# Kernel tuning notes

Measured on AMD Instinct MI355X. Metric: run time of the kernel, lower is better.

The kernel has to match this reference:

```python
import jax, jax.numpy as jnp
import numpy as np

_ALPHA_REF = 0.95
_L_REF = 96.0
GATE_THRESH = 0.7
EPS = 1e-12


def setup_inputs() -> dict:
    key = jax.random.key(0)
    ks = jax.random.split(key, 6)
    B, L, d_model = 16, 2048, 1024
    d_half = d_model // 2
    s = 1.0 / np.sqrt(d_model)
    return {
        "x": jax.random.normal(ks[0], (B, L, d_model), dtype=jnp.float32),
        "W_sem": jax.random.normal(ks[1], (d_half, d_model), dtype=jnp.float32) * s,
        "W_epi": jax.random.normal(ks[2], (d_half, d_model), dtype=jnp.float32) * s,
        "null_w": jax.random.normal(ks[3], (1, d_model), dtype=jnp.float32) * s,
        "null_b": jnp.zeros((1,), dtype=jnp.float32),
        "out_w": jax.random.normal(ks[4], (d_model, d_model), dtype=jnp.float32) * s,
        "out_b": jnp.zeros((d_model,), dtype=jnp.float32),
    }


def _normalize(v):
    # torch F.normalize: v / max(||v||, eps)
    n = jnp.linalg.norm(v, axis=-1, keepdims=True)
    return v / jnp.maximum(n, EPS)


def reference(x, W_sem, W_epi, null_w, null_b, out_w, out_b):
    B, L, d_model = x.shape
    d_half = d_model // 2
    a = _ALPHA_REF ** (_L_REF / L)  # length-adaptive EMA coefficient

    # Precompute key projections for the write steps 0..L-2: (L-1, B, d_half)
    ks_all = jnp.einsum("bld,hd->lbh", x[:, :-1, :], W_sem)
    ke_all = jnp.einsum("bld,hd->lbh", x[:, :-1, :], W_epi)
    w_all = (jnp.arange(1, L, dtype=x.dtype)) / L  # recency weights (t+1)/L

    def step(carry, inp):
        M_sem, M_epi = carry  # each (B, d_half, d_half)
        ks_t, ke_t, w_t = inp
        kns = _normalize(ks_t)
        kne = _normalize(ke_t)
        vps = jnp.einsum("bij,bj->bi", M_sem, kns)
        vpe = jnp.einsum("bij,bj->bi", M_epi, kne)
        err_s = jnp.linalg.norm(ks_t - vps, axis=-1)
        err_e = jnp.linalg.norm(ke_t - vpe, axis=-1)
        ref_s = GATE_THRESH * jnp.linalg.norm(ks_t, axis=-1)
        ref_e = GATE_THRESH * jnp.linalg.norm(ke_t, axis=-1)
        fire = ((err_s >= ref_s) | (err_e >= ref_e)).astype(x.dtype)  # (B,)
        g3 = fire[:, None, None]
        Delta_s = (ks_t - vps)[:, :, None] * kns[:, None, :]  # rank-1 outer product
        Delta_e = (ke_t - vpe)[:, :, None] * kne[:, None, :]
        M_sem = M_sem + (1.0 - a) * g3 * Delta_s
        M_epi = M_epi + (1.0 - a) * w_t * g3 * Delta_e
        return (M_sem, M_epi), None

    M0 = jnp.zeros((B, d_half, d_half), dtype=x.dtype)
    (M_sem, M_epi), _ = jax.lax.scan(step, (M0, M0), (ks_all, ke_all, w_all))

    # Query retrieval at position L-1
    q = x[:, -1, :]
    qns = _normalize(q @ W_sem.T)
    qne = _normalize(q @ W_epi.T)
    r_sem = jnp.einsum("bij,bj->bi", M_sem, qns)
    r_epi = jnp.einsum("bij,bj->bi", M_epi, qne)
    r = jnp.concatenate([r_sem, r_epi], axis=-1)  # (B, d_model)
    g_null = jax.nn.sigmoid(q @ null_w.T + null_b)  # (B, 1)
    r = g_null * r
    return r @ out_w.T + out_b
```

## Files before the change

### kernel.cpp

```cpp
#include <hip/hip_runtime.h>
#include <math.h>

#define B_    16
#define L_    2048
#define LM1   2047
#define D_    1024
#define H_    512
#define TBLK  64
#define NBLK  32

__global__ void k_proj(const float* __restrict__ x, const float* __restrict__ Wsem,
                       const float* __restrict__ Wepi, float* __restrict__ K)
{
    __shared__ float As[16][68];
    __shared__ float Bs[16][68];
    const int tid = threadIdx.x;
    const int tx = tid & 15, ty = tid >> 4;
    const int r0 = blockIdx.x * 64;
    const int n0 = blockIdx.y * 64;
    const int lr  = tid >> 2;
    const int lk4 = (tid & 3) << 2;
    const int rowg = r0 + lr;
    const bool rok = rowg < B_ * LM1;
    const int rowc = rok ? rowg : 0;
    const int bb = rowc / LM1;
    const int tt = rowc - bb * LM1;
    const float* xrow = x + ((size_t)bb * L_ + tt) * D_;
    const int nW = n0 + lr;
    const float* wrow = (nW < H_) ? (Wsem + (size_t)nW * D_)
                                  : (Wepi + (size_t)(nW - H_) * D_);
    float acc[4][4];
#pragma unroll
    for (int i = 0; i < 4; ++i)
#pragma unroll
        for (int j = 0; j < 4; ++j) acc[i][j] = 0.f;

    for (int kk = 0; kk < D_; kk += 16) {
        const float4 av = rok ? *(const float4*)(xrow + kk + lk4) : make_float4(0.f,0.f,0.f,0.f);
        const float4 bv = *(const float4*)(wrow + kk + lk4);
        As[lk4+0][lr] = av.x; As[lk4+1][lr] = av.y; As[lk4+2][lr] = av.z; As[lk4+3][lr] = av.w;
        Bs[lk4+0][lr] = bv.x; Bs[lk4+1][lr] = bv.y; Bs[lk4+2][lr] = bv.z; Bs[lk4+3][lr] = bv.w;
        __syncthreads();
#pragma unroll
        for (int k = 0; k < 16; ++k) {
            const float4 a4 = *(const float4*)&As[k][ty << 2];
            const float4 b4 = *(const float4*)&Bs[k][tx << 2];
            const float aa[4] = {a4.x, a4.y, a4.z, a4.w};
            const float bbv[4] = {b4.x, b4.y, b4.z, b4.w};
#pragma unroll
            for (int i = 0; i < 4; ++i)
#pragma unroll
                for (int j = 0; j < 4; ++j)
                    acc[i][j] = fmaf(aa[i], bbv[j], acc[i][j]);
        }
        __syncthreads();
    }
#pragma unroll
    for (int i = 0; i < 4; ++i) {
        const int r = r0 + (ty << 2) + i;
        if (r < B_ * LM1)
            *(float4*)(K + (size_t)r * D_ + n0 + (tx << 2)) =
                make_float4(acc[i][0], acc[i][1], acc[i][2], acc[i][3]);
    }
}

__global__ void k_norms(const float* __restrict__ K, float* __restrict__ nk2,
                        float* __restrict__ rn)
{
    const int r = blockIdx.x;
    const int tid = threadIdx.x;
    const float4 v = *(const float4*)(K + (size_t)r * D_ + (tid << 2));
    float s = v.x*v.x + v.y*v.y + v.z*v.z + v.w*v.w;
#pragma unroll
    for (int o = 32; o; o >>= 1) s += __shfl_xor(s, o);
    __shared__ float part[4];
    const int wid = tid >> 6, lane = tid & 63;
    if (lane == 0) part[wid] = s;
    __syncthreads();
    if (tid == 0) {
        const int b = r / LM1, t = r - b * LM1;
        const float s0 = part[0] + part[1];
        const float s1 = part[2] + part[3];
        nk2[(size_t)(b*2+0)*LM1 + t] = s0;
        nk2[(size_t)(b*2+1)*LM1 + t] = s1;
        rn [(size_t)(b*2+0)*LM1 + t] = 1.f / fmaxf(sqrtf(s0), 1e-12f);
        rn [(size_t)(b*2+1)*LM1 + t] = 1.f / fmaxf(sqrtf(s1), 1e-12f);
    }
}

__global__ void k_gram(const float* __restrict__ K, const float* __restrict__ rn,
                       float* __restrict__ G)
{
    const int blk = blockIdx.x;
    const int bm  = blockIdx.y;
    const int b = bm >> 1, m = bm & 1;
    const int t0 = blk * TBLK;
    const int Tb = (LM1 - t0 < TBLK) ? (LM1 - t0) : TBLK;
    __shared__ float As[16][68];
    const int tid = threadIdx.x;
    const int tx = tid & 15, ty = tid >> 4;
    const int lr = tid >> 2, lk4 = (tid & 3) << 2;
    const float* Abase = K + ((size_t)(b * LM1 + t0)) * D_ + m * H_;
    float acc[4][4];
#pragma unroll
    for (int i = 0; i < 4; ++i)
#pragma unroll
        for (int j = 0; j < 4; ++j) acc[i][j] = 0.f;

    for (int kk = 0; kk < H_; kk += 16) {
        const float4 av = (lr < Tb) ? *(const float4*)(Abase + (size_t)lr * D_ + kk + lk4)
                                    : make_float4(0.f,0.f,0.f,0.f);
        As[lk4+0][lr] = av.x; As[lk4+1][lr] = av.y; As[lk4+2][lr] = av.z; As[lk4+3][lr] = av.w;
        __syncthreads();
#pragma unroll
        for (int k = 0; k < 16; ++k) {
            const float4 a4 = *(const float4*)&As[k][ty << 2];
            const float4 b4 = *(const float4*)&As[k][tx << 2];
            const float aa[4] = {a4.x, a4.y, a4.z, a4.w};
            const float bbv[4] = {b4.x, b4.y, b4.z, b4.w};
#pragma unroll
            for (int i = 0; i < 4; ++i)
#pragma unroll
                for (int j = 0; j < 4; ++j)
                    acc[i][j] = fmaf(aa[i], bbv[j], acc[i][j]);
        }
        __syncthreads();
    }
    const float* rnb = rn + (size_t)bm * LM1 + t0;
    float* Gout = G + ((size_t)bm * NBLK + blk) * (TBLK * TBLK);
#pragma unroll
    for (int i = 0; i < 4; ++i) {
        const int t = (ty << 2) + i;
        const float rt = (t < Tb) ? rnb[t] : 0.f;
#pragma unroll
        for (int j = 0; j < 4; ++j) {
            const int s = (tx << 2) + j;
            const int d = s - t;
            if (d >= 0) {
                const float val = (t < Tb && s < Tb) ? rt * rnb[s] * acc[i][j] : 0.f;
                Gout[(size_t)t * TBLK + d] = val;
            }
        }
    }
}

__global__ void k_vext(const float* __restrict__ K, const float* __restrict__ M,
                       const float* __restrict__ rn, float* __restrict__ Vext,
                       int t0, int Tb)
{
    const int bm = blockIdx.y;
    const int b = bm >> 1, m = bm & 1;
    const int n0 = blockIdx.x * 64;
    __shared__ float As[16][68];
    __shared__ float Bs[16][68];
    const int tid = threadIdx.x;
    const int tx = tid & 15, ty = tid >> 4;
    const int lr = tid >> 2, lk4 = (tid & 3) << 2;
    const float* Abase = K + ((size_t)(b * LM1 + t0)) * D_ + m * H_;
    const float* Bbase = M + (size_t)bm * H_ * H_;
    float acc[4][4];
#pragma unroll
    for (int i = 0; i < 4; ++i)
#pragma unroll
        for (int j = 0; j < 4; ++j) acc[i][j] = 0.f;

    for (int kk = 0; kk < H_; kk += 16) {
        const float4 av = (lr < Tb) ? *(const float4*)(Abase + (size_t)lr * D_ + kk + lk4)
                                    : make_float4(0.f,0.f,0.f,0.f);
        const float4 bv = *(const float4*)(Bbase + (size_t)(n0 + lr) * H_ + kk + lk4);
        As[lk4+0][lr] = av.x; As[lk4+1][lr] = av.y; As[lk4+2][lr] = av.z; As[lk4+3][lr] = av.w;
        Bs[lk4+0][lr] = bv.x; Bs[lk4+1][lr] = bv.y; Bs[lk4+2][lr] = bv.z; Bs[lk4+3][lr] = bv.w;
        __syncthreads();
#pragma unroll
        for (int k = 0; k < 16; ++k) {
            const float4 a4 = *(const float4*)&As[k][ty << 2];
            const float4 b4 = *(const float4*)&Bs[k][tx << 2];
            const float aa[4] = {a4.x, a4.y, a4.z, a4.w};
            const float bbv[4] = {b4.x, b4.y, b4.z, b4.w};
#pragma unroll
            for (int i = 0; i < 4; ++i)
#pragma unroll
                for (int j = 0; j < 4; ++j)
                    acc[i][j] = fmaf(aa[i], bbv[j], acc[i][j]);
        }
        __syncthreads();
    }
    const float* rnb = rn + (size_t)bm * LM1 + t0;
#pragma unroll
    for (int i = 0; i < 4; ++i) {
        const int t = (ty << 2) + i;
        if (t < Tb) {
            const float rv = rnb[t];
            *(float4*)(Vext + ((size_t)bm * TBLK + t) * H_ + n0 + (tx << 2)) =
                make_float4(rv*acc[i][0], rv*acc[i][1], rv*acc[i][2], rv*acc[i][3]);
        }
    }
}

__global__ void __launch_bounds__(512) k_seq(
    const float* __restrict__ K, const float* __restrict__ Vext,
    const float* __restrict__ G, const float* __restrict__ nk2,
    float* __restrict__ AU, int t0, int Tb, int blk, float omA)
{
    const int b = blockIdx.x;
    const int tid = threadIdx.x;
    const int wid = tid >> 6, lane = tid & 63;
    __shared__ float Gsh[2 * TBLK * TBLK];
    __shared__ float part[32];
    {
        const float4* s0 = (const float4*)(G + ((size_t)(b*2+0) * NBLK + blk) * (TBLK*TBLK));
        const float4* s1 = (const float4*)(G + ((size_t)(b*2+1) * NBLK + blk) * (TBLK*TBLK));
        float4* dst = (float4*)Gsh;
        dst[tid]        = s0[tid];
        dst[tid + 512]  = s0[tid + 512];
        dst[tid + 1024] = s1[tid];
        dst[tid + 1536] = s1[tid + 512];
    }
    float p0[TBLK], p1[TBLK];
#pragma unroll
    for (int i = 0; i < TBLK; ++i) { p0[i] = 0.f; p1[i] = 0.f; }
    __syncthreads();

    const float* Kb0 = K + ((size_t)(b * LM1 + t0)) * D_ + tid;
    const float* Kb1 = Kb0 + H_;
    const float* Vb0 = Vext + ((size_t)(b*2+0) * TBLK) * H_ + tid;
    const float* Vb1 = Vext + ((size_t)(b*2+1) * TBLK) * H_ + tid;
    float* AU0 = AU + ((size_t)(b*2+0) * TBLK) * H_ + tid;
    float* AU1 = AU + ((size_t)(b*2+1) * TBLK) * H_ + tid;
    const float* q0 = nk2 + (size_t)(b*2+0) * LM1 + t0;
    const float* q1 = nk2 + (size_t)(b*2+1) * LM1 + t0;

    float kc0 = Kb0[0], kc1 = Kb1[0], vc0 = Vb0[0], vc1 = Vb1[0];
    float n0c = q0[0],  n1c = q1[0];

    for (int t = 0; t < Tb; ++t) {
        const float u0 = kc0 - vc0 - p0[0];
        const float u1 = kc1 - vc1 - p1[0];
        float kn0 = 0.f, kn1 = 0.f, vn0 = 0.f, vn1 = 0.f, nn0 = 0.f, nn1 = 0.f;
        if (t + 1 < Tb) {
            kn0 = Kb0[(size_t)(t+1) * D_]; kn1 = Kb1[(size_t)(t+1) * D_];
            vn0 = Vb0[(t+1) * H_];         vn1 = Vb1[(t+1) * H_];
            nn0 = q0[t+1];                 nn1 = q1[t+1];
        }
        float s0 = u0 * u0, s1 = u1 * u1;
#pragma unroll
        for (int o = 32; o; o >>= 1) { s0 += __shfl_xor(s0, o); s1 += __shfl_xor(s1, o); }
        float* pp = &part[(t & 1) << 4];
        if (lane == 0) { pp[wid] = s0; pp[wid + 8] = s1; }
        __syncthreads();
        float Ns = 0.f, Ne = 0.f;
#pragma unroll
        for (int i = 0; i < 8; ++i) { Ns += pp[i]; Ne += pp[i + 8]; }
        const bool fire = (Ns >= 0.49f * n0c) || (Ne >= 0.49f * n1c);
        const float w = (float)(t0 + t + 1) * (1.0f / (float)L_);
        const float vv0 = fire ? omA * u0 : 0.f;
        const float vv1 = fire ? omA * w * u1 : 0.f;
        AU0[(size_t)t * H_] = vv0;
        AU1[(size_t)t * H_] = vv1;
        const float* g0 = Gsh + t * TBLK;
        const float* g1 = Gsh + (TBLK + t) * TBLK;
        if (fire) {
#pragma unroll
            for (int q = 0; q < 16; ++q) {
                const float4 a = ((const float4*)g0)[q];
                const float4 c = ((const float4*)g1)[q];
                const int d0 = q << 2;
                if (q > 0) { p0[d0-1] = fmaf(a.x, vv0, p0[d0]); p1[d0-1] = fmaf(c.x, vv1, p1[d0]); }
                p0[d0+0] = fmaf(a.y, vv0, p0[d0+1]);  p1[d0+0] = fmaf(c.y, vv1, p1[d0+1]);
                p0[d0+1] = fmaf(a.z, vv0, p0[d0+2]);  p1[d0+1] = fmaf(c.z, vv1, p1[d0+2]);
                p0[d0+2] = fmaf(a.w, vv0, p0[d0+3]);  p1[d0+2] = fmaf(c.w, vv1, p1[d0+3]);
            }
        } else {
#pragma unroll
            for (int d = 1; d < TBLK; ++d) { p0[d-1] = p0[d]; p1[d-1] = p1[d]; }
        }
        p0[TBLK-1] = 0.f; p1[TBLK-1] = 0.f;
        kc0 = kn0; kc1 = kn1; vc0 = vn0; vc1 = vn1; n0c = nn0; n1c = nn1;
    }
}

__global__ void k_update(const float* __restrict__ AU, const float* __restrict__ K,
                         const float* __restrict__ rn, float* __restrict__ M,
                         int t0, int Tb)
{
    const int bm = blockIdx.y;
    const int b = bm >> 1, m = bm & 1;
    const int i0 = (blockIdx.x >> 3) * 64;
    const int j0 = (blockIdx.x & 7) * 64;
    __shared__ float As[16][68];
    __shared__ float Bs[16][68];
    const int tid = threadIdx.x;
    const int tx = tid & 15, ty = tid >> 4;
    const int lk = tid >> 4;
    const int lc4 = (tid & 15) << 2;
    float acc[4][4];
#pragma unroll
    for (int i = 0; i < 4; ++i)
#pragma unroll
        for (int j = 0; j < 4; ++j) acc[i][j] = 0.f;

    for (int kk = 0; kk < TBLK; kk += 16) {
        const int kt = kk + lk;
        const bool ok = kt < Tb;
        float4 av = ok ? *(const float4*)(AU + ((size_t)bm * TBLK + kt) * H_ + i0 + lc4)
                       : make_float4(0.f,0.f,0.f,0.f);
        const float rv = ok ? rn[(size_t)bm * LM1 + t0 + kt] : 0.f;
        float4 bv = ok ? *(const float4*)(K + ((size_t)(b * LM1 + t0 + kt)) * D_ + m * H_ + j0 + lc4)
                       : make_float4(0.f,0.f,0.f,0.f);
        bv.x *= rv; bv.y *= rv; bv.z *= rv; bv.w *= rv;
        *(float4*)&As[lk][lc4] = av;
        *(float4*)&Bs[lk][lc4] = bv;
        __syncthreads();
#pragma unroll
        for (int k = 0; k < 16; ++k) {
            const float4 a4 = *(const float4*)&As[k][ty << 2];
            const float4 b4 = *(const float4*)&Bs[k][tx << 2];
            const float aa[4] = {a4.x, a4.y, a4.z, a4.w};
            const float bbv[4] = {b4.x, b4.y, b4.z, b4.w};
#pragma unroll
            for (int i = 0; i < 4; ++i)
#pragma unroll
                for (int j = 0; j < 4; ++j)
                    acc[i][j] = fmaf(aa[i], bbv[j], acc[i][j]);
        }
        __syncthreads();
    }
#pragma unroll
    for (int i = 0; i < 4; ++i) {
        float4* p = (float4*)(M + ((size_t)bm * H_ + i0 + (ty << 2) + i) * H_ + j0 + (tx << 2));
        float4 old = *p;
        old.x += acc[i][0]; old.y += acc[i][1]; old.z += acc[i][2]; old.w += acc[i][3];
        *p = old;
    }
}

__global__ void __launch_bounds__(1024) k_q(
    const float* __restrict__ x, const float* __restrict__ Wsem,
    const float* __restrict__ Wepi, const float* __restrict__ nw,
    const float* __restrict__ nb, float* __restrict__ qn, float* __restrict__ gnull)
{
    const int b = blockIdx.x, tid = threadIdx.x;
    __shared__ float qsh[D_];
    __shared__ float red[16];
    qsh[tid] = x[((size_t)b * L_ + (L_ - 1)) * D_ + tid];
    __syncthreads();
    const float* wrow = (tid < H_) ? (Wsem + (size_t)tid * D_)
                                   : (Wepi + (size_t)(tid - H_) * D_);
    float s = 0.f;
    for (int d = 0; d < D_; d += 4) {
        const float4 w4 = *(const float4*)(wrow + d);
        s += qsh[d]*w4.x + qsh[d+1]*w4.y + qsh[d+2]*w4.z + qsh[d+3]*w4.w;
    }
    float sq = s * s;
#pragma unroll
    for (int o = 32; o; o >>= 1) sq += __shfl_xor(sq, o);
    const int wid = tid >> 6, lane = tid & 63;
    if (lane == 0) red[wid] = sq;
    __syncthreads();
    float n2s = 0.f, n2e = 0.f;
#pragma unroll
    for (int i = 0; i < 8; ++i) { n2s += red[i]; n2e += red[i + 8]; }
    const float rns = 1.f / fmaxf(sqrtf(n2s), 1e-12f);
    const float rne = 1.f / fmaxf(sqrtf(n2e), 1e-12f);
    qn[(size_t)b * D_ + tid] = s * ((tid < H_) ? rns : rne);
    if (wid == 0) {
        float g = 0.f;
        for (int d = lane * 4; d < D_; d += 256) {
            const float4 w4 = *(const float4*)(nw + d);
            g += qsh[d]*w4.x + qsh[d+1]*w4.y + qsh[d+2]*w4.z + qsh[d+3]*w4.w;
        }
#pragma unroll
        for (int o = 32; o; o >>= 1) g += __shfl_xor(g, o);
        if (lane == 0) gnull[b] = 1.f / (1.f + expf(-(g + nb[0])));
    }
}

__global__ void k_rmv(const float* __restrict__ M, const float* __restrict__ qn,
                      const float* __restrict__ gnull, float* __restrict__ rg)
{
    const int b = blockIdx.x;
    const int n = blockIdx.y * 4 + (threadIdx.x >> 6);
    const int lane = threadIdx.x & 63;
    const int m = n >> 9, i = n & 511;
    const float* Mr = M + ((size_t)(b*2+m) * H_ + i) * H_;
    const float* qv = qn + (size_t)b * D_ + m * H_;
    float s = 0.f;
#pragma unroll
    for (int it = 0; it < 2; ++it) {
        const int j = lane * 4 + it * 256;
        const float4 m4 = *(const float4*)(Mr + j);
        const float4 q4 = *(const float4*)(qv + j);
        s += m4.x*q4.x + m4.y*q4.y + m4.z*q4.z + m4.w*q4.w;
    }
#pragma unroll
    for (int o = 32; o; o >>= 1) s += __shfl_xor(s, o);
    if (lane == 0) rg[(size_t)b * D_ + n] = gnull[b] * s;
}

__global__ void k_out(const float* __restrict__ rg, const float* __restrict__ outw,
                      const float* __restrict__ outb, float* __restrict__ out)
{
    const int b = blockIdx.x;
    const int o = blockIdx.y * 4 + (threadIdx.x >> 6);
    const int lane = threadIdx.x & 63;
    const float* wr = outw + (size_t)o * D_;
    const float* rv = rg + (size_t)b * D_;
    float s = 0.f;
#pragma unroll
    for (int it = 0; it < 4; ++it) {
        const int j = lane * 4 + it * 256;
        const float4 w4 = *(const float4*)(wr + j);
        const float4 r4 = *(const float4*)(rv + j);
        s += w4.x*r4.x + w4.y*r4.y + w4.z*r4.z + w4.w*r4.w;
    }
#pragma unroll
    for (int o2 = 32; o2; o2 >>= 1) s += __shfl_xor(s, o2);
    if (lane == 0) out[(size_t)b * D_ + o] = s + outb[o];
}

extern "C" void kernel_launch(void* const* d_in, const int* in_sizes, int n_in,
                              void* d_out, int out_size, void* d_ws, size_t ws_size,
                              hipStream_t stream)
{
    (void)in_sizes; (void)n_in; (void)out_size;
    const float* x     = (const float*)d_in[0];
    const float* Wsem  = (const float*)d_in[1];
    const float* Wepi  = (const float*)d_in[2];
    const float* nullw = (const float*)d_in[3];
    const float* nullb = (const float*)d_in[4];
    const float* outw  = (const float*)d_in[5];
    const float* outb  = (const float*)d_in[6];
    float* out = (float*)d_out;

    float* ws = (float*)d_ws;
    size_t off = 0;
    float* K     = ws + off; off += (size_t)B_ * LM1 * D_;
    float* nk2   = ws + off; off += (size_t)B_ * 2 * LM1;
    float* rn    = ws + off; off += (size_t)B_ * 2 * LM1;
    float* Mm    = ws + off; off += (size_t)B_ * 2 * H_ * H_;
    float* Vext  = ws + off; off += (size_t)B_ * 2 * TBLK * H_;
    float* G     = ws + off; off += (size_t)B_ * 2 * NBLK * TBLK * TBLK;
    float* AU    = ws + off; off += (size_t)B_ * 2 * TBLK * H_;
    float* qn    = ws + off; off += (size_t)B_ * D_;
    float* gnull = ws + off; off += (size_t)B_;
    float* rg    = ws + off; off += (size_t)B_ * D_;
    if (ws_size < off * sizeof(float)) return;

    const float omA = (float)(1.0 - pow(0.95, 96.0 / 2048.0));

    hipMemsetAsync(Mm, 0, (size_t)B_ * 2 * H_ * H_ * sizeof(float), stream);

    k_proj <<<dim3(512, 16), 256, 0, stream>>>(x, Wsem, Wepi, K);
    k_norms<<<dim3(B_ * LM1), 256, 0, stream>>>(K, nk2, rn);
    k_gram <<<dim3(NBLK, B_ * 2), 256, 0, stream>>>(K, rn, G);

    for (int blk = 0; blk < NBLK; ++blk) {
        const int t0 = blk * TBLK;
        const int Tb = (LM1 - t0 < TBLK) ? (LM1 - t0) : TBLK;
        k_vext  <<<dim3(8, B_ * 2), 256, 0, stream>>>(K, Mm, rn, Vext, t0, Tb);
        k_seq   <<<dim3(B_), 512, 0, stream>>>(K, Vext, G, nk2, AU, t0, Tb, blk, omA);
        k_update<<<dim3(64, B_ * 2), 256, 0, stream>>>(AU, K, rn, Mm, t0, Tb);
    }

    k_q  <<<dim3(B_), 1024, 0, stream>>>(x, Wsem, Wepi, nullw, nullb, qn, gnull);
    k_rmv<<<dim3(16, 256), 256, 0, stream>>>(Mm, qn, gnull, rg);
    k_out<<<dim3(16, 256), 256, 0, stream>>>(rg, outw, outb, out);
}
```

Before: 7.000 ms.

## Fuse per-block vext/seq/update launches into one persistent cooperative kernel

Replaces the 96 per-chunk kernel launches (vext, seq, update across 32 chunks) and the memset with a single cooperative persistent kernel of 256 workgroups that uses grid.sync between phases. The vext GEMM is split-K across two 256-thread halves with a shared-memory reduction, and the update GEMM tiles are distributed across all workgroups. This removes launch overhead and inter-kernel gaps, at the cost of grid-wide barriers and only 16 workgroups being busy during the sequential phase.

```diff
diff --git a/kernel.cpp b/kernel.cpp
--- a/kernel.cpp
+++ b/kernel.cpp
@@ -1,5 +1,8 @@
 #include <hip/hip_runtime.h>
+#include <hip/hip_cooperative_groups.h>
 #include <math.h>
+
+namespace cg = cooperative_groups;
 
 #define B_    16
 #define L_    2048
@@ -8,6 +11,7 @@
 #define H_    512
 #define TBLK  64
 #define NBLK  32
+#define NWG   256
 
 __global__ void k_proj(const float* __restrict__ x, const float* __restrict__ Wsem,
                        const float* __restrict__ Wepi, float* __restrict__ K)
@@ -144,193 +148,224 @@
     }
 }
 
-__global__ void k_vext(const float* __restrict__ K, const float* __restrict__ M,
-                       const float* __restrict__ rn, float* __restrict__ Vext,
-                       int t0, int Tb)
-{
-    const int bm = blockIdx.y;
-    const int b = bm >> 1, m = bm & 1;
-    const int n0 = blockIdx.x * 64;
-    __shared__ float As[16][68];
-    __shared__ float Bs[16][68];
+__global__ void __launch_bounds__(512, 2) k_scan(
+    const float* __restrict__ K, const float* __restrict__ rn,
+    const float* __restrict__ nk2, const float* __restrict__ G,
+    float* __restrict__ Mm, float* __restrict__ Vext, float* __restrict__ AU,
+    float omA)
+{
+    cg::grid_group grid = cg::this_grid();
+    const int wg  = blockIdx.x;
     const int tid = threadIdx.x;
-    const int tx = tid & 15, ty = tid >> 4;
-    const int lr = tid >> 2, lk4 = (tid & 3) << 2;
-    const float* Abase = K + ((size_t)(b * LM1 + t0)) * D_ + m * H_;
-    const float* Bbase = M + (size_t)bm * H_ * H_;
-    float acc[4][4];
-#pragma unroll
-    for (int i = 0; i < 4; ++i)
-#pragma unroll
-        for (int j = 0; j < 4; ++j) acc[i][j] = 0.f;
-
-    for (int kk = 0; kk < H_; kk += 16) {
-        const float4 av = (lr < Tb) ? *(const float4*)(Abase + (size_t)lr * D_ + kk + lk4)
-                                    : make_float4(0.f,0.f,0.f,0.f);
-        const float4 bv = *(const float4*)(Bbase + (size_t)(n0 + lr) * H_ + kk + lk4);
-        As[lk4+0][lr] = av.x; As[lk4+1][lr] = av.y; As[lk4+2][lr] = av.z; As[lk4+3][lr] = av.w;
-        Bs[lk4+0][lr] = bv.x; Bs[lk4+1][lr] = bv.y; Bs[lk4+2][lr] = bv.z; Bs[lk4+3][lr] = bv.w;
-        __syncthreads();
-#pragma unroll
-        for (int k = 0; k < 16; ++k) {
-            const float4 a4 = *(const float4*)&As[k][ty << 2];
-            const float4 b4 = *(const float4*)&Bs[k][tx << 2];
-            const float aa[4] = {a4.x, a4.y, a4.z, a4.w};
-            const float bbv[4] = {b4.x, b4.y, b4.z, b4.w};
+    __shared__ float sh[8448];
+    __shared__ float part[32];
+
+    {
+        float4* M4 = (float4*)Mm;
+        for (int i = wg * 512 + tid; i < (B_*2*H_*H_) / 4; i += NWG * 512)
+            M4[i] = make_float4(0.f, 0.f, 0.f, 0.f);
+    }
+    grid.sync();
+
+    for (int blk = 0; blk < NBLK; ++blk) {
+        const int t0 = blk * TBLK;
+        const int Tb = (LM1 - t0 < TBLK) ? (LM1 - t0) : TBLK;
+
+        {
+            const int sub = tid >> 8, t256 = tid & 255;
+            float* As = sh + sub * 2176;
+            float* Bs = As + 1088;
+            float* Cred = sh + 4352;
+            const int bm = wg >> 3, n0 = (wg & 7) << 6;
+            const int b = bm >> 1, m = bm & 1;
+            const int tx = t256 & 15, ty = t256 >> 4;
+            const int lr = t256 >> 2, lk4 = (t256 & 3) << 2;
+            const float* Abase = K + ((size_t)(b * LM1 + t0)) * D_ + m * H_ + sub * 256;
+            const float* Bbase = Mm + (size_t)bm * H_ * H_ + sub * 256;
+            float acc[4][4];
 #pragma unroll
             for (int i = 0; i < 4; ++i)
 #pragma unroll
-                for (int j = 0; j < 4; ++j)
-                    acc[i][j] = fmaf(aa[i], bbv[j], acc[i][j]);
-        }
-        __syncthreads();
-    }
-    const float* rnb = rn + (size_t)bm * LM1 + t0;
-#pragma unroll
-    for (int i = 0; i < 4; ++i) {
-        const int t = (ty << 2) + i;
-        if (t < Tb) {
-            const float rv = rnb[t];
-            *(float4*)(Vext + ((size_t)bm * TBLK + t) * H_ + n0 + (tx << 2)) =
-                make_float4(rv*acc[i][0], rv*acc[i][1], rv*acc[i][2], rv*acc[i][3]);
-        }
-    }
-}
-
-__global__ void __launch_bounds__(512) k_seq(
-    const float* __restrict__ K, const float* __restrict__ Vext,
-    const float* __restrict__ G, const float* __restrict__ nk2,
-    float* __restrict__ AU, int t0, int Tb, int blk, float omA)
-{
-    const int b = blockIdx.x;
-    const int tid = threadIdx.x;
-    const int wid = tid >> 6, lane = tid & 63;
-    __shared__ float Gsh[2 * TBLK * TBLK];
-    __shared__ float part[32];
-    {
-        const float4* s0 = (const float4*)(G + ((size_t)(b*2+0) * NBLK + blk) * (TBLK*TBLK));
-        const float4* s1 = (const float4*)(G + ((size_t)(b*2+1) * NBLK + blk) * (TBLK*TBLK));
-        float4* dst = (float4*)Gsh;
-        dst[tid]        = s0[tid];
-        dst[tid + 512]  = s0[tid + 512];
-        dst[tid + 1024] = s1[tid];
-        dst[tid + 1536] = s1[tid + 512];
-    }
-    float p0[TBLK], p1[TBLK];
-#pragma unroll
-    for (int i = 0; i < TBLK; ++i) { p0[i] = 0.f; p1[i] = 0.f; }
-    __syncthreads();
-
-    const float* Kb0 = K + ((size_t)(b * LM1 + t0)) * D_ + tid;
-    const float* Kb1 = Kb0 + H_;
-    const float* Vb0 = Vext + ((size_t)(b*2+0) * TBLK) * H_ + tid;
-    const float* Vb1 = Vext + ((size_t)(b*2+1) * TBLK) * H_ + tid;
-    float* AU0 = AU + ((size_t)(b*2+0) * TBLK) * H_ + tid;
-    float* AU1 = AU + ((size_t)(b*2+1) * TBLK) * H_ + tid;
-    const float* q0 = nk2 + (size_t)(b*2+0) * LM1 + t0;
-    const float* q1 = nk2 + (size_t)(b*2+1) * LM1 + t0;
-
-    float kc0 = Kb0[0], kc1 = Kb1[0], vc0 = Vb0[0], vc1 = Vb1[0];
-    float n0c = q0[0],  n1c = q1[0];
-
-    for (int t = 0; t < Tb; ++t) {
-        const float u0 = kc0 - vc0 - p0[0];
-        const float u1 = kc1 - vc1 - p1[0];
-        float kn0 = 0.f, kn1 = 0.f, vn0 = 0.f, vn1 = 0.f, nn0 = 0.f, nn1 = 0.f;
-        if (t + 1 < Tb) {
-            kn0 = Kb0[(size_t)(t+1) * D_]; kn1 = Kb1[(size_t)(t+1) * D_];
-            vn0 = Vb0[(t+1) * H_];         vn1 = Vb1[(t+1) * H_];
-            nn0 = q0[t+1];                 nn1 = q1[t+1];
-        }
-        float s0 = u0 * u0, s1 = u1 * u1;
-#pragma unroll
-        for (int o = 32; o; o >>= 1) { s0 += __shfl_xor(s0, o); s1 += __shfl_xor(s1, o); }
-        float* pp = &part[(t & 1) << 4];
-        if (lane == 0) { pp[wid] = s0; pp[wid + 8] = s1; }
-        __syncthreads();
-        float Ns = 0.f, Ne = 0.f;
-#pragma unroll
-        for (int i = 0; i < 8; ++i) { Ns += pp[i]; Ne += pp[i + 8]; }
-        const bool fire = (Ns >= 0.49f * n0c) || (Ne >= 0.49f * n1c);
-        const float w = (float)(t0 + t + 1) * (1.0f / (float)L_);
-        const float vv0 = fire ? omA * u0 : 0.f;
-        const float vv1 = fire ? omA * w * u1 : 0.f;
-        AU0[(size_t)t * H_] = vv0;
-        AU1[(size_t)t * H_] = vv1;
-        const float* g0 = Gsh + t * TBLK;
-        const float* g1 = Gsh + (TBLK + t) * TBLK;
-        if (fire) {
-#pragma unroll
-            for (int q = 0; q < 16; ++q) {
-                const float4 a = ((const float4*)g0)[q];
-                const float4 c = ((const float4*)g1)[q];
-                const int d0 = q << 2;
-                if (q > 0) { p0[d0-1] = fmaf(a.x, vv0, p0[d0]); p1[d0-1] = fmaf(c.x, vv1, p1[d0]); }
-                p0[d0+0] = fmaf(a.y, vv0, p0[d0+1]);  p1[d0+0] = fmaf(c.y, vv1, p1[d0+1]);
-                p0[d0+1] = fmaf(a.z, vv0, p0[d0+2]);  p1[d0+1] = fmaf(c.z, vv1, p1[d0+2]);
-                p0[d0+2] = fmaf(a.w, vv0, p0[d0+3]);  p1[d0+2] = fmaf(c.w, vv1, p1[d0+3]);
-            }
-        } else {
-#pragma unroll
-            for (int d = 1; d < TBLK; ++d) { p0[d-1] = p0[d]; p1[d-1] = p1[d]; }
-        }
-        p0[TBLK-1] = 0.f; p1[TBLK-1] = 0.f;
-        kc0 = kn0; kc1 = kn1; vc0 = vn0; vc1 = vn1; n0c = nn0; n1c = nn1;
-    }
-}
-
-__global__ void k_update(const float* __restrict__ AU, const float* __restrict__ K,
-                         const float* __restrict__ rn, float* __restrict__ M,
-                         int t0, int Tb)
-{
-    const int bm = blockIdx.y;
-    const int b = bm >> 1, m = bm & 1;
-    const int i0 = (blockIdx.x >> 3) * 64;
-    const int j0 = (blockIdx.x & 7) * 64;
-    __shared__ float As[16][68];
-    __shared__ float Bs[16][68];
-    const int tid = threadIdx.x;
-    const int tx = tid & 15, ty = tid >> 4;
-    const int lk = tid >> 4;
-    const int lc4 = (tid & 15) << 2;
-    float acc[4][4];
-#pragma unroll
-    for (int i = 0; i < 4; ++i)
-#pragma unroll
-        for (int j = 0; j < 4; ++j) acc[i][j] = 0.f;
-
-    for (int kk = 0; kk < TBLK; kk += 16) {
-        const int kt = kk + lk;
-        const bool ok = kt < Tb;
-        float4 av = ok ? *(const float4*)(AU + ((size_t)bm * TBLK + kt) * H_ + i0 + lc4)
-                       : make_float4(0.f,0.f,0.f,0.f);
-        const float rv = ok ? rn[(size_t)bm * LM1 + t0 + kt] : 0.f;
-        float4 bv = ok ? *(const float4*)(K + ((size_t)(b * LM1 + t0 + kt)) * D_ + m * H_ + j0 + lc4)
-                       : make_float4(0.f,0.f,0.f,0.f);
-        bv.x *= rv; bv.y *= rv; bv.z *= rv; bv.w *= rv;
-        *(float4*)&As[lk][lc4] = av;
-        *(float4*)&Bs[lk][lc4] = bv;
-        __syncthreads();
-#pragma unroll
-        for (int k = 0; k < 16; ++k) {
-            const float4 a4 = *(const float4*)&As[k][ty << 2];
-            const float4 b4 = *(const float4*)&Bs[k][tx << 2];
-            const float aa[4] = {a4.x, a4.y, a4.z, a4.w};
-            const float bbv[4] = {b4.x, b4.y, b4.z, b4.w};
-#pragma unroll
-            for (int i = 0; i < 4; ++i)
-#pragma unroll
-                for (int j = 0; j < 4; ++j)
-                    acc[i][j] = fmaf(aa[i], bbv[j], acc[i][j]);
-        }
-        __syncthreads();
-    }
-#pragma unroll
-    for (int i = 0; i < 4; ++i) {
-        float4* p = (float4*)(M + ((size_t)bm * H_ + i0 + (ty << 2) + i) * H_ + j0 + (tx << 2));
-        float4 old = *p;
-        old.x += acc[i][0]; old.y += acc[i][1]; old.z += acc[i][2]; old.w += acc[i][3];
-        *p = old;
+                for (int j = 0; j < 4; ++j) acc[i][j] = 0.f;
+
+            for (int kk = 0; kk < 256; kk += 16) {
+                const float4 av = (lr < Tb) ? *(const float4*)(Abase + (size_t)lr * D_ + kk + lk4)
+                                            : make_float4(0.f,0.f,0.f,0.f);
+                const float4 bv = *(const float4*)(Bbase + (size_t)(n0 + lr) * H_ + kk + lk4);
+                As[(lk4+0)*68 + lr] = av.x; As[(lk4+1)*68 + lr] = av.y;
+                As[(lk4+2)*68 + lr] = av.z; As[(lk4+3)*68 + lr] = av.w;
+                Bs[(lk4+0)*68 + lr] = bv.x; Bs[(lk4+1)*68 + lr] = bv.y;
+                Bs[(lk4+2)*68 + lr] = bv.z; Bs[(lk4+3)*68 + lr] = bv.w;
+                __syncthreads();
+#pragma unroll
+                for (int k = 0; k < 16; ++k) {
+                    const float4 a4 = *(const float4*)&As[k*68 + (ty << 2)];
+                    const float4 b4 = *(const float4*)&Bs[k*68 + (tx << 2)];
+                    const float aa[4] = {a4.x, a4.y, a4.z, a4.w};
+                    const float bbv[4] = {b4.x, b4.y, b4.z, b4.w};
+#pragma unroll
+                    for (int i = 0; i < 4; ++i)
+#pragma unroll
+                        for (int j = 0; j < 4; ++j)
+                            acc[i][j] = fmaf(aa[i], bbv[j], acc[i][j]);
+                }
+                __syncthreads();
+            }
+            if (sub == 1) {
+#pragma unroll
+                for (int i = 0; i < 4; ++i)
+#pragma unroll
+                    for (int j = 0; j < 4; ++j)
+                        Cred[((size_t)((ty << 2) + i) << 6) + (tx << 2) + j] = acc[i][j];
+            }
+            __syncthreads();
+            if (sub == 0) {
+                const float* rnb = rn + (size_t)bm * LM1 + t0;
+#pragma unroll
+                for (int i = 0; i < 4; ++i) {
+                    const int t = (ty << 2) + i;
+                    if (t < Tb) {
+                        const float rv = rnb[t];
+                        const float* cr = &Cred[((size_t)t << 6) + (tx << 2)];
+                        *(float4*)(Vext + ((size_t)bm * TBLK + t) * H_ + n0 + (tx << 2)) =
+                            make_float4(rv*(acc[i][0]+cr[0]), rv*(acc[i][1]+cr[1]),
+                                        rv*(acc[i][2]+cr[2]), rv*(acc[i][3]+cr[3]));
+                    }
+                }
+            }
+        }
+        grid.sync();
+
+        if (wg < B_) {
+            const int b = wg;
+            const int wid = tid >> 6, lane = tid & 63;
+            {
+                const float4* s0 = (const float4*)(G + ((size_t)(b*2+0) * NBLK + blk) * (TBLK*TBLK));
+                const float4* s1 = (const float4*)(G + ((size_t)(b*2+1) * NBLK + blk) * (TBLK*TBLK));
+                float4* dst = (float4*)sh;
+                dst[tid]        = s0[tid];
+                dst[tid + 512]  = s0[tid + 512];
+                dst[tid + 1024] = s1[tid];
+                dst[tid + 1536] = s1[tid + 512];
+            }
+            float p0[TBLK], p1[TBLK];
+#pragma unroll
+            for (int i = 0; i < TBLK; ++i) { p0[i] = 0.f; p1[i] = 0.f; }
+            __syncthreads();
+
+            const float* Kb0 = K + ((size_t)(b * LM1 + t0)) * D_ + tid;
+            const float* Kb1 = Kb0 + H_;
+            const float* Vb0 = Vext + ((size_t)(b*2+0) * TBLK) * H_ + tid;
+            const float* Vb1 = Vext + ((size_t)(b*2+1) * TBLK) * H_ + tid;
+            float* AU0 = AU + ((size_t)(b*2+0) * TBLK) * H_ + tid;
+            float* AU1 = AU + ((size_t)(b*2+1) * TBLK) * H_ + tid;
+            const float* q0 = nk2 + (size_t)(b*2+0) * LM1 + t0;
+            const float* q1 = nk2 + (size_t)(b*2+1) * LM1 + t0;
+
+            float kc0 = Kb0[0], kc1 = Kb1[0], vc0 = Vb0[0], vc1 = Vb1[0];
+            float n0c = q0[0],  n1c = q1[0];
+
+            for (int t = 0; t < Tb; ++t) {
+                const float u0 = kc0 - vc0 - p0[0];
+                const float u1 = kc1 - vc1 - p1[0];
+                float kn0 = 0.f, kn1 = 0.f, vn0 = 0.f, vn1 = 0.f, nn0 = 0.f, nn1 = 0.f;
+                if (t + 1 < Tb) {
+                    kn0 = Kb0[(size_t)(t+1) * D_]; kn1 = Kb1[(size_t)(t+1) * D_];
+                    vn0 = Vb0[(t+1) * H_];         vn1 = Vb1[(t+1) * H_];
+                    nn0 = q0[t+1];                 nn1 = q1[t+1];
+                }
+                float s0 = u0 * u0, s1 = u1 * u1;
+#pragma unroll
+                for (int o = 32; o; o >>= 1) { s0 += __shfl_xor(s0, o); s1 += __shfl_xor(s1, o); }
+                float* pp = &part[(t & 1) << 4];
+                if (lane == 0) { pp[wid] = s0; pp[wid + 8] = s1; }
+                __syncthreads();
+                float Ns = 0.f, Ne = 0.f;
+#pragma unroll
+                for (int i = 0; i < 8; ++i) { Ns += pp[i]; Ne += pp[i + 8]; }
+                const bool fire = (Ns >= 0.49f * n0c) || (Ne >= 0.49f * n1c);
+                const float w = (float)(t0 + t + 1) * (1.0f / (float)L_);
+                const float vv0 = fire ? omA * u0 : 0.f;
+                const float vv1 = fire ? omA * w * u1 : 0.f;
+                AU0[(size_t)t * H_] = vv0;
+                AU1[(size_t)t * H_] = vv1;
+                const float* g0 = sh + t * TBLK;
+                const float* g1 = sh + (TBLK + t) * TBLK;
+                if (fire) {
+#pragma unroll
+                    for (int q = 0; q < 16; ++q) {
+                        const float4 a = ((const float4*)g0)[q];
+                        const float4 c = ((const float4*)g1)[q];
+                        const int d0 = q << 2;
+                        if (q > 0) { p0[d0-1] = fmaf(a.x, vv0, p0[d0]); p1[d0-1] = fmaf(c.x, vv1, p1[d0]); }
+                        p0[d0+0] = fmaf(a.y, vv0, p0[d0+1]);  p1[d0+0] = fmaf(c.y, vv1, p1[d0+1]);
+                        p0[d0+1] = fmaf(a.z, vv0, p0[d0+2]);  p1[d0+1] = fmaf(c.z, vv1, p1[d0+2]);
+                        p0[d0+2] = fmaf(a.w, vv0, p0[d0+3]);  p1[d0+2] = fmaf(c.w, vv1, p1[d0+3]);
+                    }
+                } else {
+#pragma unroll
+                    for (int d = 1; d < TBLK; ++d) { p0[d-1] = p0[d]; p1[d-1] = p1[d]; }
+                }
+                p0[TBLK-1] = 0.f; p1[TBLK-1] = 0.f;
+                kc0 = kn0; kc1 = kn1; vc0 = vn0; vc1 = vn1; n0c = nn0; n1c = nn1;
+            }
+        }
+        grid.sync();
+
+        {
+            const int sub = tid >> 8, t256 = tid & 255;
+            float* As = sh + sub * 2176;
+            float* Bs = As + 1088;
+            const int tx = t256 & 15, ty = t256 >> 4;
+            const int lk = t256 >> 4, lc4 = (t256 & 15) << 2;
+            for (int q = 0; q < 4; ++q) {
+                const int task = q * 512 + wg * 2 + sub;
+                const int bm = task >> 6;
+                const int i0 = ((task >> 3) & 7) << 6;
+                const int j0 = (task & 7) << 6;
+                const int b = bm >> 1, m = bm & 1;
+                float acc[4][4];
+#pragma unroll
+                for (int i = 0; i < 4; ++i)
+#pragma unroll
+                    for (int j = 0; j < 4; ++j) acc[i][j] = 0.f;
+
+                for (int kk = 0; kk < TBLK; kk += 16) {
+                    const int kt = kk + lk;
+                    const bool ok = kt < Tb;
+                    float4 av = ok ? *(const float4*)(AU + ((size_t)bm * TBLK + kt) * H_ + i0 + lc4)
+                                   : make_float4(0.f,0.f,0.f,0.f);
+                    const float rv = ok ? rn[(size_t)bm * LM1 + t0 + kt] : 0.f;
+                    float4 bv = ok ? *(const float4*)(K + ((size_t)(b * LM1 + t0 + kt)) * D_ + m * H_ + j0 + lc4)
+                                   : make_float4(0.f,0.f,0.f,0.f);
+                    bv.x *= rv; bv.y *= rv; bv.z *= rv; bv.w *= rv;
+                    *(float4*)&As[lk*68 + lc4] = av;
+                    *(float4*)&Bs[lk*68 + lc4] = bv;
+                    __syncthreads();
+#pragma unroll
+                    for (int k = 0; k < 16; ++k) {
+                        const float4 a4 = *(const float4*)&As[k*68 + (ty << 2)];
+                        const float4 b4 = *(const float4*)&Bs[k*68 + (tx << 2)];
+                        const float aa[4] = {a4.x, a4.y, a4.z, a4.w};
+                        const float bbv[4] = {b4.x, b4.y, b4.z, b4.w};
+#pragma unroll
+                        for (int i = 0; i < 4; ++i)
+#pragma unroll
+                            for (int j = 0; j < 4; ++j)
+                                acc[i][j] = fmaf(aa[i], bbv[j], acc[i][j]);
+                    }
+                    __syncthreads();
+                }
+#pragma unroll
+                for (int i = 0; i < 4; ++i) {
+                    float4* p = (float4*)(Mm + ((size_t)bm * H_ + i0 + (ty << 2) + i) * H_ + j0 + (tx << 2));
+                    float4 old = *p;
+                    old.x += acc[i][0]; old.y += acc[i][1]; old.z += acc[i][2]; old.w += acc[i][3];
+                    *p = old;
+                }
+            }
+        }
+        grid.sync();
     }
 }
 
@@ -446,20 +481,16 @@
     float* rg    = ws + off; off += (size_t)B_ * D_;
     if (ws_size < off * sizeof(float)) return;
 
-    const float omA = (float)(1.0 - pow(0.95, 96.0 / 2048.0));
-
-    hipMemsetAsync(Mm, 0, (size_t)B_ * 2 * H_ * H_ * sizeof(float), stream);
+    float omA = (float)(1.0 - pow(0.95, 96.0 / 2048.0));
 
     k_proj <<<dim3(512, 16), 256, 0, stream>>>(x, Wsem, Wepi, K);
     k_norms<<<dim3(B_ * LM1), 256, 0, stream>>>(K, nk2, rn);
     k_gram <<<dim3(NBLK, B_ * 2), 256, 0, stream>>>(K, rn, G);
 
-    for (int blk = 0; blk < NBLK; ++blk) {
-        const int t0 = blk * TBLK;
-        const int Tb = (LM1 - t0 < TBLK) ? (LM1 - t0) : TBLK;
-        k_vext  <<<dim3(8, B_ * 2), 256, 0, stream>>>(K, Mm, rn, Vext, t0, Tb);
-        k_seq   <<<dim3(B_), 512, 0, stream>>>(K, Vext, G, nk2, AU, t0, Tb, blk, omA);
-        k_update<<<dim3(64, B_ * 2), 256, 0, stream>>>(AU, K, rn, Mm, t0, Tb);
+    {
+        void* args[] = { (void*)&K, (void*)&rn, (void*)&nk2, (void*)&G,
+                         (void*)&Mm, (void*)&Vext, (void*)&AU, (void*)&omA };
+        hipLaunchCooperativeKernel((void*)k_scan, dim3(NWG), dim3(512), args, 0, stream);
     }
 
     k_q  <<<dim3(B_), 1024, 0, stream>>>(x, Wsem, Wepi, nullw, nullb, qn, gnull);
```

Result: slower. 9.770 ms (+39.6%).
